# Kernel tuning notes

Hardware: AMD Instinct MI355X
Metric: run time of the kernel (lower is better)

## Reference

```python
import jax, jax.numpy as jnp
import numpy as np

N = 100000
E = 1600000
IN_FEATS = 512
N_HIDDEN = 128
N_CLASSES = 40


def setup_inputs() -> dict:
    key = jax.random.key(0)
    k1, k2, k3, k4, k5, k6, k7 = jax.random.split(key, 7)
    inputs = jax.random.normal(k1, (N, IN_FEATS), dtype=jnp.float32)
    edge_index = jax.random.randint(k2, (2, E), 0, N, dtype=jnp.int64)
    edge_attr = jax.random.uniform(k3, (E,), dtype=jnp.float32)
    # GCNConv params (Glorot-ish scaling)
    W1 = jax.random.normal(k4, (IN_FEATS, N_HIDDEN), dtype=jnp.float32) / np.sqrt(IN_FEATS)
    b1 = jnp.zeros((N_HIDDEN,), dtype=jnp.float32)
    W2 = jax.random.normal(k5, (N_HIDDEN, N_CLASSES), dtype=jnp.float32) / np.sqrt(N_HIDDEN)
    b2 = jnp.zeros((N_CLASSES,), dtype=jnp.float32)
    return {"inputs": inputs, "edge_index": edge_index, "edge_attr": edge_attr,
            "W1": W1, "b1": b1, "W2": W2, "b2": b2}


def gcn_conv(x, W, b, src, dst, edge_weight):
    """GCNConv with normalize=False: linear transform, then edge-weighted
    scatter-sum from src to dst, then bias."""
    m = x @ W                                   # [N, F_out]
    msgs = m[src] * edge_weight[:, None]        # gather + weight, [E, F_out]
    agg = jax.ops.segment_sum(msgs, dst, num_segments=x.shape[0])  # scatter-add
    return agg + b


def reference(inputs, edge_index, edge_attr, W1, b1, W2, b2):
    src, dst = edge_index[0], edge_index[1]
    h = jax.nn.relu(gcn_conv(inputs, W1, b1, src, dst, edge_attr))
    # F.dropout with training=False (eval mode) is identity -> deterministic baseline
    preds = gcn_conv(h, W2, b2, src, dst, edge_attr)
    return jax.nn.log_softmax(preds, axis=1)
```

## Files before the change

kernel.cpp:

```cpp
#include <hip/hip_runtime.h>
#include <hip/hip_bf16.h>
#include <cstdint>

#define N_NODES 100000
#define N_EDGES 1600000
#define F_IN    512
#define F_HID   128
#define F_OUT   40
#define F_OUT_PAD 48

#define BSH    8
#define NB     391
#define BEPT   8
#define BCHUNK 4096
#define GB     391
#define CONVB  140
#define FCAP   6144

typedef short v8s __attribute__((ext_vector_type(8)));
typedef float v4f __attribute__((ext_vector_type(4)));

__device__ __forceinline__ short f2bf(float f) {
    unsigned u = __float_as_uint(f);
    u += 0x7fffu + ((u >> 16) & 1u);
    return (short)(u >> 16);
}

__device__ __forceinline__ float bflo(unsigned u) { return __uint_as_float(u << 16); }
__device__ __forceinline__ float bfhi(unsigned u) { return __uint_as_float(u & 0xffff0000u); }

__device__ __forceinline__ v8s pack8(float4 a, float4 b) {
    v8s r;
    r[0] = f2bf(a.x); r[1] = f2bf(a.y); r[2] = f2bf(a.z); r[3] = f2bf(a.w);
    r[4] = f2bf(b.x); r[5] = f2bf(b.y); r[6] = f2bf(b.z); r[7] = f2bf(b.w);
    return r;
}

__device__ __forceinline__ void gload16(const void* g, void* l) {
    __builtin_amdgcn_global_load_lds(
        (const __attribute__((address_space(1))) void*)g,
        (__attribute__((address_space(3))) void*)l, 16, 0, 0);
}


__global__ __launch_bounds__(512) void k_bhist(const int* __restrict__ dst,
                                               int* __restrict__ bcnt,
                                               const float* __restrict__ W1,
                                               short* __restrict__ WT1,
                                               const float* __restrict__ W2,
                                               short* __restrict__ WT2) {
    if (blockIdx.x >= GB) {
        int i = (blockIdx.x - GB) * 512 + threadIdx.x;
        if (i < F_IN * F_HID) {
            int n = i >> 9, k = i & 511;
            WT1[i] = f2bf(W1[k * F_HID + n]);
        } else {
            int j = i - F_IN * F_HID;
            if (j < F_OUT_PAD * F_HID) {
                int n = j >> 7, k = j & 127;
                WT2[j] = (n < F_OUT) ? f2bf(W2[k * F_OUT + n]) : (short)0;
            }
        }
        return;
    }
    __shared__ int lh[512];
    int tid = threadIdx.x;
    lh[tid] = 0;
    __syncthreads();
    long e0 = (long)blockIdx.x * BCHUNK;
#pragma unroll
    for (int i = 0; i < BEPT; i++) {
        long e = e0 + tid + i * 512;
        if (e < N_EDGES) atomicAdd(&lh[dst[e] >> BSH], 1);
    }
    __syncthreads();
    if (tid < NB && lh[tid]) atomicAdd(&bcnt[tid], lh[tid]);
}

__global__ __launch_bounds__(512) void k_bscan(const int* __restrict__ bcnt,
                                               int* __restrict__ bbase,
                                               int* __restrict__ bcur) {
    __shared__ int sm[512];
    int tid = threadIdx.x;
    int v = (tid < NB) ? bcnt[tid] : 0;
    sm[tid] = v;
    __syncthreads();
    for (int off = 1; off < 512; off <<= 1) {
        int t = (tid >= off) ? sm[tid - off] : 0;
        __syncthreads();
        sm[tid] += t;
        __syncthreads();
    }
    if (tid < NB) {
        int ex = sm[tid] - v;
        bbase[tid] = ex;
        bcur[tid] = ex;
    }
    if (tid == 511) bbase[NB] = sm[511];
}

__global__ __launch_bounds__(512) void k_bscatter(const int* __restrict__ src,
                                                  const int* __restrict__ dst,
                                                  const float* __restrict__ w,
                                                  int* __restrict__ bcur,
                                                  int2* __restrict__ tmp) {
    __shared__ int cntA[512];
    __shared__ int ofsA[512];
    __shared__ int lcur[512];
    __shared__ int gb[512];
    __shared__ __align__(16) int2 recBuf[BCHUNK];
    __shared__ unsigned short bkt[BCHUNK];
    int tid = threadIdx.x;
    long e0 = (long)blockIdx.x * BCHUNK;
    cntA[tid] = 0;
    __syncthreads();

    int dloc[BEPT];
#pragma unroll
    for (int i = 0; i < BEPT; i++) {
        long e = e0 + tid + i * 512;
        int d = (e < N_EDGES) ? dst[e] : -1;
        dloc[i] = d;
        if (d >= 0) atomicAdd(&cntA[d >> BSH], 1);
    }
    __syncthreads();

    int v = cntA[tid];
    ofsA[tid] = v;
    __syncthreads();
    for (int off = 1; off < 512; off <<= 1) {
        int t = (tid >= off) ? ofsA[tid - off] : 0;
        __syncthreads();
        ofsA[tid] += t;
        __syncthreads();
    }
    int excl = ofsA[tid] - v;
    ofsA[tid] = excl;
    lcur[tid] = excl;
    if (tid < NB && v > 0) gb[tid] = atomicAdd(&bcur[tid], v);
    __syncthreads();

#pragma unroll
    for (int i = 0; i < BEPT; i++) {
        int d = dloc[i];
        if (d >= 0) {
            long e = e0 + tid + i * 512;
            int j = d >> BSH;
            int slot = atomicAdd(&lcur[j], 1);
            recBuf[slot] = make_int2(src[e] | ((d & 255) << 17), __float_as_int(w[e]));
            bkt[slot] = (unsigned short)j;
        }
    }
    __syncthreads();

    long rem = N_EDGES - e0;
    int total = (rem < BCHUNK) ? (int)rem : BCHUNK;
    for (int s = tid; s < total; s += 512) {
        int j = bkt[s];
        tmp[gb[j] + (s - ofsA[j])] = recBuf[s];
    }
}

__global__ __launch_bounds__(256) void k_fine(const int2* __restrict__ tmp,
                                              const int* __restrict__ bbase,
                                              int2* __restrict__ rec,
                                              int* __restrict__ rowptr,
                                              int* __restrict__ deg) {
    __shared__ int hist[256];
    __shared__ int ofs[256];
    __shared__ int cur[256];
    __shared__ __align__(16) int2 recOut[FCAP];
    int tid = threadIdx.x, b = blockIdx.x;
    int base = bbase[b];
    int cnt = bbase[b + 1] - base;

    hist[tid] = 0;
    __syncthreads();
    for (int i = tid; i < cnt; i += 256) {
        unsigned u = (unsigned)tmp[base + i].x;
        atomicAdd(&hist[u >> 17], 1);
    }
    __syncthreads();

    int v = hist[tid];
    ofs[tid] = v;
    __syncthreads();
    for (int off = 1; off < 256; off <<= 1) {
        int t = (tid >= off) ? ofs[tid - off] : 0;
        __syncthreads();
        ofs[tid] += t;
        __syncthreads();
    }
    int excl = ofs[tid] - v;
    ofs[tid] = excl;
    cur[tid] = excl;
    int node = (b << BSH) + tid;
    if (node < N_NODES) {
        rowptr[node] = base + excl;
        deg[node] = v;
    }
    __syncthreads();

    if (cnt <= FCAP) {
        for (int i = tid; i < cnt; i += 256) {
            int2 r = tmp[base + i];
            unsigned u = (unsigned)r.x;
            int slot = atomicAdd(&cur[u >> 17], 1);
            recOut[slot] = make_int2((int)(u & 0x1FFFFu), r.y);
        }
        __syncthreads();
        for (int i = tid; i < cnt; i += 256) rec[base + i] = recOut[i];
    } else {
        for (int i = tid; i < cnt; i += 256) {
            int2 r = tmp[base + i];
            unsigned u = (unsigned)r.x;
            int slot = atomicAdd(&cur[u >> 17], 1);
            rec[base + slot] = make_int2((int)(u & 0x1FFFFu), r.y);
        }
    }
}


__global__ __launch_bounds__(256) void k_gemm1(const float* __restrict__ x,
                                               const short* __restrict__ WT1,
                                               unsigned short* __restrict__ m1b) {
    __shared__ __align__(16) float aBuf[2][64 * 32];
    __shared__ __align__(16) short bBuf[2][128 * 32];
    int tid = threadIdx.x, w = tid >> 6, lane = tid & 63;
    int quad = lane >> 4, l16 = lane & 15;
    long rowBase = (long)blockIdx.x * 64;

    int ar = lane >> 3, ac = lane & 7;
    int br = lane >> 2, bc = lane & 3;

    v4f acc[8];
#pragma unroll
    for (int t = 0; t < 8; t++) acc[t] = (v4f){0.f, 0.f, 0.f, 0.f};

    auto stage = [&](int kc, int buf) {
#pragma unroll
        for (int i = 0; i < 2; i++) {
            int rl = w * 16 + i * 8 + ar;
            long rg = rowBase + rl;
            if (rg > N_NODES - 1) rg = N_NODES - 1;
            const float* gp = x + rg * F_IN + kc * 32 + ((ac ^ (rl & 7)) << 2);
            gload16(gp, &aBuf[buf][(w * 16 + i * 8) * 32]);
        }
#pragma unroll
        for (int i = 0; i < 2; i++) {
            int n = w * 32 + i * 16 + br;
            const short* gp = WT1 + n * F_IN + kc * 32 + ((bc ^ ((n >> 1) & 3)) << 3);
            gload16(gp, &bBuf[buf][(w * 32 + i * 16) * 32]);
        }
    };

    stage(0, 0);
#pragma unroll
    for (int kc = 0; kc < 16; kc++) {
        __syncthreads();
        int buf = kc & 1;
        if (kc < 15) stage(kc + 1, buf ^ 1);
        int arow = w * 16 + l16;
        int p0 = (2 * quad) ^ (l16 & 7);
        float4 av0 = *(const float4*)&aBuf[buf][arow * 32 + p0 * 4];
        float4 av1 = *(const float4*)&aBuf[buf][arow * 32 + (p0 ^ 1) * 4];
        v8s af = pack8(av0, av1);
#pragma unroll
        for (int t = 0; t < 8; t++) {
            int n = t * 16 + l16;
            int p = quad ^ ((n >> 1) & 3);
            v8s bf = *(const v8s*)&bBuf[buf][n * 32 + p * 8];
            acc[t] = __builtin_amdgcn_mfma_f32_16x16x32_bf16(af, bf, acc[t], 0, 0, 0);
        }
    }

#pragma unroll
    for (int t = 0; t < 8; t++)
#pragma unroll
        for (int r = 0; r < 4; r++) {
            long row = rowBase + w * 16 + quad * 4 + r;
            if (row < N_NODES)
                m1b[row * F_HID + t * 16 + l16] = (unsigned short)f2bf(acc[t][r]);
        }
}


__global__ __launch_bounds__(256) void k_ag(const int2* __restrict__ rec,
                                            const int* __restrict__ rowptr,
                                            const int* __restrict__ deg,
                                            const uint4* __restrict__ m1v,
                                            const float* __restrict__ b1,
                                            const short* __restrict__ WT2,
                                            unsigned short* __restrict__ m2b) {
    __shared__ uint4 ht[4][16][16];
    int tid = threadIdx.x, w = tid >> 6, lane = tid & 63;
    int q = lane >> 4, l16 = lane & 15;
    int gBase = (blockIdx.x * 4 + w) * 16;

    int idx = gBase + l16;
    int rp = 0, dg = 0;
    if (idx < N_NODES) { rp = rowptr[idx]; dg = deg[idx]; }
    const float4* b4 = (const float4*)b1;
    float4 bv0 = b4[2 * l16], bv1 = b4[2 * l16 + 1];

    for (int i = 0; i < 16; i++) {
        int start = __shfl(rp, i);
        int cnt = __shfl(dg, i);
        float a0 = 0.f, a1 = 0.f, a2 = 0.f, a3 = 0.f;
        float a4 = 0.f, a5 = 0.f, a6 = 0.f, a7 = 0.f;
        int e = start + q;
        int n16 = cnt >> 4;
        for (int k = 0; k < n16; k++) {
            int2 r0 = rec[e];
            int2 r1 = rec[e + 4];
            int2 r2 = rec[e + 8];
            int2 r3 = rec[e + 12];
            uint4 g0 = m1v[(long)r0.x * 16 + l16];
            uint4 g1 = m1v[(long)r1.x * 16 + l16];
            uint4 g2 = m1v[(long)r2.x * 16 + l16];
            uint4 g3 = m1v[(long)r3.x * 16 + l16];
            float w0 = __int_as_float(r0.y), w1 = __int_as_float(r1.y);
            float w2 = __int_as_float(r2.y), w3 = __int_as_float(r3.y);
            a0 = fmaf(w0, bflo(g0.x), a0); a1 = fmaf(w0, bfhi(g0.x), a1);
            a2 = fmaf(w0, bflo(g0.y), a2); a3 = fmaf(w0, bfhi(g0.y), a3);
            a4 = fmaf(w0, bflo(g0.z), a4); a5 = fmaf(w0, bfhi(g0.z), a5);
            a6 = fmaf(w0, bflo(g0.w), a6); a7 = fmaf(w0, bfhi(g0.w), a7);
            a0 = fmaf(w1, bflo(g1.x), a0); a1 = fmaf(w1, bfhi(g1.x), a1);
            a2 = fmaf(w1, bflo(g1.y), a2); a3 = fmaf(w1, bfhi(g1.y), a3);
            a4 = fmaf(w1, bflo(g1.z), a4); a5 = fmaf(w1, bfhi(g1.z), a5);
            a6 = fmaf(w1, bflo(g1.w), a6); a7 = fmaf(w1, bfhi(g1.w), a7);
            a0 = fmaf(w2, bflo(g2.x), a0); a1 = fmaf(w2, bfhi(g2.x), a1);
            a2 = fmaf(w2, bflo(g2.y), a2); a3 = fmaf(w2, bfhi(g2.y), a3);
            a4 = fmaf(w2, bflo(g2.z), a4); a5 = fmaf(w2, bfhi(g2.z), a5);
            a6 = fmaf(w2, bflo(g2.w), a6); a7 = fmaf(w2, bfhi(g2.w), a7);
            a0 = fmaf(w3, bflo(g3.x), a0); a1 = fmaf(w3, bfhi(g3.x), a1);
            a2 = fmaf(w3, bflo(g3.y), a2); a3 = fmaf(w3, bfhi(g3.y), a3);
            a4 = fmaf(w3, bflo(g3.z), a4); a5 = fmaf(w3, bfhi(g3.z), a5);
            a6 = fmaf(w3, bflo(g3.w), a6); a7 = fmaf(w3, bfhi(g3.w), a7);
            e += 16;
        }
        if (cnt & 8) {
            int2 r0 = rec[e];
            int2 r1 = rec[e + 4];
            uint4 g0 = m1v[(long)r0.x * 16 + l16];
            uint4 g1 = m1v[(long)r1.x * 16 + l16];
            float w0 = __int_as_float(r0.y), w1 = __int_as_float(r1.y);
            a0 = fmaf(w0, bflo(g0.x), a0); a1 = fmaf(w0, bfhi(g0.x), a1);
            a2 = fmaf(w0, bflo(g0.y), a2); a3 = fmaf(w0, bfhi(g0.y), a3);
            a4 = fmaf(w0, bflo(g0.z), a4); a5 = fmaf(w0, bfhi(g0.z), a5);
            a6 = fmaf(w0, bflo(g0.w), a6); a7 = fmaf(w0, bfhi(g0.w), a7);
            a0 = fmaf(w1, bflo(g1.x), a0); a1 = fmaf(w1, bfhi(g1.x), a1);
            a2 = fmaf(w1, bflo(g1.y), a2); a3 = fmaf(w1, bfhi(g1.y), a3);
            a4 = fmaf(w1, bflo(g1.z), a4); a5 = fmaf(w1, bfhi(g1.z), a5);
            a6 = fmaf(w1, bflo(g1.w), a6); a7 = fmaf(w1, bfhi(g1.w), a7);
            e += 8;
        }
        for (int t = e; t < start + cnt; t += 4) {
            int2 r = rec[t];
            uint4 g = m1v[(long)r.x * 16 + l16];
            float ww = __int_as_float(r.y);
            a0 = fmaf(ww, bflo(g.x), a0); a1 = fmaf(ww, bfhi(g.x), a1);
            a2 = fmaf(ww, bflo(g.y), a2); a3 = fmaf(ww, bfhi(g.y), a3);
            a4 = fmaf(ww, bflo(g.z), a4); a5 = fmaf(ww, bfhi(g.z), a5);
            a6 = fmaf(ww, bflo(g.w), a6); a7 = fmaf(ww, bfhi(g.w), a7);
        }
        a0 += __shfl_xor(a0, 16); a0 += __shfl_xor(a0, 32);
        a1 += __shfl_xor(a1, 16); a1 += __shfl_xor(a1, 32);
        a2 += __shfl_xor(a2, 16); a2 += __shfl_xor(a2, 32);
        a3 += __shfl_xor(a3, 16); a3 += __shfl_xor(a3, 32);
        a4 += __shfl_xor(a4, 16); a4 += __shfl_xor(a4, 32);
        a5 += __shfl_xor(a5, 16); a5 += __shfl_xor(a5, 32);
        a6 += __shfl_xor(a6, 16); a6 += __shfl_xor(a6, 32);
        a7 += __shfl_xor(a7, 16); a7 += __shfl_xor(a7, 32);
        if (q == 0) {
            a0 = fmaxf(a0 + bv0.x, 0.f); a1 = fmaxf(a1 + bv0.y, 0.f);
            a2 = fmaxf(a2 + bv0.z, 0.f); a3 = fmaxf(a3 + bv0.w, 0.f);
            a4 = fmaxf(a4 + bv1.x, 0.f); a5 = fmaxf(a5 + bv1.y, 0.f);
            a6 = fmaxf(a6 + bv1.z, 0.f); a7 = fmaxf(a7 + bv1.w, 0.f);
            uint4 o;
            o.x = (unsigned)(unsigned short)f2bf(a0) | ((unsigned)(unsigned short)f2bf(a1) << 16);
            o.y = (unsigned)(unsigned short)f2bf(a2) | ((unsigned)(unsigned short)f2bf(a3) << 16);
            o.z = (unsigned)(unsigned short)f2bf(a4) | ((unsigned)(unsigned short)f2bf(a5) << 16);
            o.w = (unsigned)(unsigned short)f2bf(a6) | ((unsigned)(unsigned short)f2bf(a7) << 16);
            ht[w][i][l16 ^ (i & 7)] = o;
        }
    }

    v4f acc[3];
#pragma unroll
    for (int t = 0; t < 3; t++) acc[t] = (v4f){0.f, 0.f, 0.f, 0.f};
#pragma unroll
    for (int kk = 0; kk < 4; kk++) {
        uint4 av = ht[w][l16][(kk * 4 + q) ^ (l16 & 7)];
        v8s af = *reinterpret_cast<const v8s*>(&av);
        const short* brow = WT2 + l16 * F_HID + q * 8 + kk * 32;
#pragma unroll
        for (int t = 0; t < 3; t++) {
            v8s bf = *reinterpret_cast<const v8s*>(brow + t * 16 * F_HID);
            acc[t] = __builtin_amdgcn_mfma_f32_16x16x32_bf16(af, bf, acc[t], 0, 0, 0);
        }
    }
#pragma unroll
    for (int r = 0; r < 4; r++) {
        int g = gBase + q * 4 + r;
        if (g < N_NODES) {
#pragma unroll
            for (int t = 0; t < 3; t++)
                m2b[(long)g * 64 + t * 16 + l16] = (unsigned short)f2bf(acc[t][r]);
            m2b[(long)g * 64 + 48 + l16] = 0;
        }
    }
}


__global__ void k_agg2(const int2* __restrict__ rec, const int* __restrict__ rowptr,
                       const int* __restrict__ deg, const uint4* __restrict__ m2v,
                       const float* __restrict__ b2, float* __restrict__ out) {
    int node = blockIdx.x * 4 + (threadIdx.x >> 6);
    int lane = threadIdx.x & 63;
    if (node >= N_NODES) return;
    int start = rowptr[node], cnt = deg[node];
    int oc = lane >> 3, l8 = lane & 7;

    float a0 = 0.f, a1 = 0.f, a2 = 0.f, a3 = 0.f;
    float a4 = 0.f, a5 = 0.f, a6 = 0.f, a7 = 0.f;

    int e = start + oc;
    int n16 = cnt >> 4;
    for (int k = 0; k < n16; k++) {
        int2 r0 = rec[e];
        int2 r1 = rec[e + 8];
        uint4 g0 = m2v[(long)r0.x * 8 + l8];
        uint4 g1 = m2v[(long)r1.x * 8 + l8];
        float w0 = __int_as_float(r0.y), w1 = __int_as_float(r1.y);
        a0 = fmaf(w0, bflo(g0.x), a0); a1 = fmaf(w0, bfhi(g0.x), a1);
        a2 = fmaf(w0, bflo(g0.y), a2); a3 = fmaf(w0, bfhi(g0.y), a3);
        a4 = fmaf(w0, bflo(g0.z), a4); a5 = fmaf(w0, bfhi(g0.z), a5);
        a6 = fmaf(w0, bflo(g0.w), a6); a7 = fmaf(w0, bfhi(g0.w), a7);
        a0 = fmaf(w1, bflo(g1.x), a0); a1 = fmaf(w1, bfhi(g1.x), a1);
        a2 = fmaf(w1, bflo(g1.y), a2); a3 = fmaf(w1, bfhi(g1.y), a3);
        a4 = fmaf(w1, bflo(g1.z), a4); a5 = fmaf(w1, bfhi(g1.z), a5);
        a6 = fmaf(w1, bflo(g1.w), a6); a7 = fmaf(w1, bfhi(g1.w), a7);
        e += 16;
    }
    if (cnt & 8) {
        int2 r = rec[e];
        uint4 g = m2v[(long)r.x * 8 + l8];
        float w = __int_as_float(r.y);
        a0 = fmaf(w, bflo(g.x), a0); a1 = fmaf(w, bfhi(g.x), a1);
        a2 = fmaf(w, bflo(g.y), a2); a3 = fmaf(w, bfhi(g.y), a3);
        a4 = fmaf(w, bflo(g.z), a4); a5 = fmaf(w, bfhi(g.z), a5);
        a6 = fmaf(w, bflo(g.w), a6); a7 = fmaf(w, bfhi(g.w), a7);
        e += 8;
    }
    if (e < start + cnt) {
        int2 r = rec[e];
        uint4 g = m2v[(long)r.x * 8 + l8];
        float w = __int_as_float(r.y);
        a0 = fmaf(w, bflo(g.x), a0); a1 = fmaf(w, bfhi(g.x), a1);
        a2 = fmaf(w, bflo(g.y), a2); a3 = fmaf(w, bfhi(g.y), a3);
        a4 = fmaf(w, bflo(g.z), a4); a5 = fmaf(w, bfhi(g.z), a5);
        a6 = fmaf(w, bflo(g.w), a6); a7 = fmaf(w, bfhi(g.w), a7);
    }
#pragma unroll
    for (int off = 8; off < 64; off <<= 1) {
        a0 += __shfl_xor(a0, off); a1 += __shfl_xor(a1, off);
        a2 += __shfl_xor(a2, off); a3 += __shfl_xor(a3, off);
        a4 += __shfl_xor(a4, off); a5 += __shfl_xor(a5, off);
        a6 += __shfl_xor(a6, off); a7 += __shfl_xor(a7, off);
    }

    const float NEG = -3.4e38f;
    float v0 = NEG, v1 = NEG, v2 = NEG, v3 = NEG;
    float v4 = NEG, v5 = NEG, v6 = NEG, v7 = NEG;
    if (l8 < 5) {
        const float4* b4 = (const float4*)b2;
        float4 bv0 = b4[2 * l8], bv1 = b4[2 * l8 + 1];
        v0 = a0 + bv0.x; v1 = a1 + bv0.y; v2 = a2 + bv0.z; v3 = a3 + bv0.w;
        v4 = a4 + bv1.x; v5 = a5 + bv1.y; v6 = a6 + bv1.z; v7 = a7 + bv1.w;
    }
    float m = fmaxf(fmaxf(fmaxf(v0, v1), fmaxf(v2, v3)),
                    fmaxf(fmaxf(v4, v5), fmaxf(v6, v7)));
#pragma unroll
    for (int off = 1; off < 8; off <<= 1) m = fmaxf(m, __shfl_xor(m, off));
    float s = 0.f;
    if (l8 < 5)
        s = __expf(v0 - m) + __expf(v1 - m) + __expf(v2 - m) + __expf(v3 - m) +
            __expf(v4 - m) + __expf(v5 - m) + __expf(v6 - m) + __expf(v7 - m);
#pragma unroll
    for (int off = 1; off < 8; off <<= 1) s += __shfl_xor(s, off);
    if (oc == 0 && l8 < 5) {
        float ls = m + __logf(s);
        float4* op = (float4*)(out + (long)node * F_OUT);
        float4 o0, o1;
        o0.x = v0 - ls; o0.y = v1 - ls; o0.z = v2 - ls; o0.w = v3 - ls;
        o1.x = v4 - ls; o1.y = v5 - ls; o1.z = v6 - ls; o1.w = v7 - ls;
        op[2 * l8] = o0;
        op[2 * l8 + 1] = o1;
    }
}


extern "C" void kernel_launch(void* const* d_in, const int* in_sizes, int n_in,
                              void* d_out, int out_size, void* d_ws, size_t ws_size,
                              hipStream_t stream) {
    const float* x  = (const float*)d_in[0];
    const int* ei   = (const int*)d_in[1];
    const int* src  = ei;
    const int* dst  = ei + N_EDGES;
    const float* ew = (const float*)d_in[2];
    const float* W1 = (const float*)d_in[3];
    const float* b1 = (const float*)d_in[4];
    const float* W2 = (const float*)d_in[5];
    const float* b2 = (const float*)d_in[6];
    float* out = (float*)d_out;

    char* ws = (char*)d_ws;
    size_t off = 0;
    auto alloc = [&](size_t bytes) {
        void* p = ws + off;
        off += (bytes + 255) & ~(size_t)255;
        return p;
    };
    unsigned short* m1b  = (unsigned short*)alloc((size_t)N_NODES * F_HID * 2);
    unsigned short* m2b  = (unsigned short*)alloc((size_t)N_NODES * 64 * 2);
    int2*           rec  = (int2*)alloc((size_t)N_EDGES * 8);
    int*          rowptr = (int*)alloc((size_t)N_NODES * 4);
    int*          deg    = (int*)alloc((size_t)N_NODES * 4);
    int*          bCnt   = (int*)alloc(512 * 4);
    int*          bBase  = (int*)alloc(512 * 4);
    int*          bCur   = (int*)alloc(512 * 4);
    short*        WT1    = (short*)alloc((size_t)F_HID * F_IN * 2);
    short*        WT2    = (short*)alloc((size_t)F_OUT_PAD * F_HID * 2);

    int2* tmp = (int2*)m2b;

    hipMemsetAsync(bCnt, 0, 512 * 4, stream);

    k_bhist<<<GB + CONVB, 512, 0, stream>>>(dst, bCnt, W1, WT1, W2, WT2);
    k_bscan<<<1, 512, 0, stream>>>(bCnt, bBase, bCur);
    k_bscatter<<<GB, 512, 0, stream>>>(src, dst, ew, bCur, tmp);
    k_fine<<<NB, 256, 0, stream>>>(tmp, bBase, rec, rowptr, deg);

    k_gemm1<<<(N_NODES + 63) / 64, 256, 0, stream>>>(x, WT1, m1b);
    k_ag<<<(N_NODES + 63) / 64, 256, 0, stream>>>(rec, rowptr, deg,
                                                  (const uint4*)m1b, b1, WT2, m2b);
    k_agg2<<<(N_NODES + 3) / 4, 256, 0, stream>>>(rec, rowptr, deg,
                                                  (const uint4*)m2b, b2, out);
}
```

Measured before the change: 491.0 us.

## Spread layer-1 aggregation across 8 waves per 16-node block, pack rowptr/deg

The layer-1 aggregation kernel is restructured. Before, each wave serially aggregated 16 nodes and then ran its own small MFMA; now a 512-thread block handles 16 nodes, with each of 8 waves aggregating 2 nodes into shared memory, and after a barrier a single wave does the W2 MFMA. The aim is more parallelism and latency hiding on the irregular gathers and less serial per-wave work. Row pointers and degrees are also packed into one int2 array so each node needs a single load. The cost is a block barrier and seven idle waves during the MFMA/store phase.

```diff
diff --git a/kernel.cpp b/kernel.cpp
--- a/kernel.cpp
+++ b/kernel.cpp
@@ -164,8 +164,7 @@
 __global__ __launch_bounds__(256) void k_fine(const int2* __restrict__ tmp,
                                               const int* __restrict__ bbase,
                                               int2* __restrict__ rec,
-                                              int* __restrict__ rowptr,
-                                              int* __restrict__ deg) {
+                                              int2* __restrict__ rd) {
     __shared__ int hist[256];
     __shared__ int ofs[256];
     __shared__ int cur[256];
@@ -195,10 +194,7 @@
     ofs[tid] = excl;
     cur[tid] = excl;
     int node = (b << BSH) + tid;
-    if (node < N_NODES) {
-        rowptr[node] = base + excl;
-        deg[node] = v;
-    }
+    if (node < N_NODES) rd[node] = make_int2(base + excl, v);
     __syncthreads();
 
     if (cnt <= FCAP) {
@@ -285,27 +281,27 @@
 }
 
 
-__global__ __launch_bounds__(256) void k_ag(const int2* __restrict__ rec,
-                                            const int* __restrict__ rowptr,
-                                            const int* __restrict__ deg,
+__global__ __launch_bounds__(512) void k_ag(const int2* __restrict__ rec,
+                                            const int2* __restrict__ rd,
                                             const uint4* __restrict__ m1v,
                                             const float* __restrict__ b1,
                                             const short* __restrict__ WT2,
                                             unsigned short* __restrict__ m2b) {
-    __shared__ uint4 ht[4][16][16];
+    __shared__ uint4 ht[16][17];
     int tid = threadIdx.x, w = tid >> 6, lane = tid & 63;
     int q = lane >> 4, l16 = lane & 15;
-    int gBase = (blockIdx.x * 4 + w) * 16;
-
-    int idx = gBase + l16;
-    int rp = 0, dg = 0;
-    if (idx < N_NODES) { rp = rowptr[idx]; dg = deg[idx]; }
+    int gBase = blockIdx.x * 16;
+
     const float4* b4 = (const float4*)b1;
     float4 bv0 = b4[2 * l16], bv1 = b4[2 * l16 + 1];
 
-    for (int i = 0; i < 16; i++) {
-        int start = __shfl(rp, i);
-        int cnt = __shfl(dg, i);
+#pragma unroll
+    for (int half = 0; half < 2; half++) {
+        int node = gBase + half * 8 + w;
+        int2 sd = make_int2(0, 0);
+        if (node < N_NODES) sd = rd[node];
+        int start = sd.x, cnt = sd.y;
+
         float a0 = 0.f, a1 = 0.f, a2 = 0.f, a3 = 0.f;
         float a4 = 0.f, a5 = 0.f, a6 = 0.f, a7 = 0.f;
         int e = start + q;
@@ -382,44 +378,48 @@
             o.y = (unsigned)(unsigned short)f2bf(a2) | ((unsigned)(unsigned short)f2bf(a3) << 16);
             o.z = (unsigned)(unsigned short)f2bf(a4) | ((unsigned)(unsigned short)f2bf(a5) << 16);
             o.w = (unsigned)(unsigned short)f2bf(a6) | ((unsigned)(unsigned short)f2bf(a7) << 16);
-            ht[w][i][l16 ^ (i & 7)] = o;
-        }
-    }
-
-    v4f acc[3];
-#pragma unroll
-    for (int t = 0; t < 3; t++) acc[t] = (v4f){0.f, 0.f, 0.f, 0.f};
-#pragma unroll
-    for (int kk = 0; kk < 4; kk++) {
-        uint4 av = ht[w][l16][(kk * 4 + q) ^ (l16 & 7)];
-        v8s af = *reinterpret_cast<const v8s*>(&av);
-        const short* brow = WT2 + l16 * F_HID + q * 8 + kk * 32;
-#pragma unroll
-        for (int t = 0; t < 3; t++) {
-            v8s bf = *reinterpret_cast<const v8s*>(brow + t * 16 * F_HID);
-            acc[t] = __builtin_amdgcn_mfma_f32_16x16x32_bf16(af, bf, acc[t], 0, 0, 0);
-        }
-    }
-#pragma unroll
-    for (int r = 0; r < 4; r++) {
-        int g = gBase + q * 4 + r;
-        if (g < N_NODES) {
-#pragma unroll
-            for (int t = 0; t < 3; t++)
-                m2b[(long)g * 64 + t * 16 + l16] = (unsigned short)f2bf(acc[t][r]);
-            m2b[(long)g * 64 + 48 + l16] = 0;
-        }
-    }
-}
-
-
-__global__ void k_agg2(const int2* __restrict__ rec, const int* __restrict__ rowptr,
-                       const int* __restrict__ deg, const uint4* __restrict__ m2v,
-                       const float* __restrict__ b2, float* __restrict__ out) {
+            ht[half * 8 + w][l16] = o;
+        }
+    }
+    __syncthreads();
+
+    if (w == 0) {
+        v4f acc[3];
+#pragma unroll
+        for (int t = 0; t < 3; t++) acc[t] = (v4f){0.f, 0.f, 0.f, 0.f};
+#pragma unroll
+        for (int kk = 0; kk < 4; kk++) {
+            uint4 av = ht[l16][kk * 4 + q];
+            v8s af = *reinterpret_cast<const v8s*>(&av);
+            const short* brow = WT2 + l16 * F_HID + q * 8 + kk * 32;
+#pragma unroll
+            for (int t = 0; t < 3; t++) {
+                v8s bf = *reinterpret_cast<const v8s*>(brow + t * 16 * F_HID);
+                acc[t] = __builtin_amdgcn_mfma_f32_16x16x32_bf16(af, bf, acc[t], 0, 0, 0);
+            }
+        }
+#pragma unroll
+        for (int r = 0; r < 4; r++) {
+            int g = gBase + q * 4 + r;
+            if (g < N_NODES) {
+#pragma unroll
+                for (int t = 0; t < 3; t++)
+                    m2b[(long)g * 64 + t * 16 + l16] = (unsigned short)f2bf(acc[t][r]);
+                m2b[(long)g * 64 + 48 + l16] = 0;
+            }
+        }
+    }
+}
+
+
+__global__ void k_agg2(const int2* __restrict__ rec, const int2* __restrict__ rd,
+                       const uint4* __restrict__ m2v, const float* __restrict__ b2,
+                       float* __restrict__ out) {
     int node = blockIdx.x * 4 + (threadIdx.x >> 6);
     int lane = threadIdx.x & 63;
     if (node >= N_NODES) return;
-    int start = rowptr[node], cnt = deg[node];
+    int2 sd = rd[node];
+    int start = sd.x, cnt = sd.y;
     int oc = lane >> 3, l8 = lane & 7;
 
     float a0 = 0.f, a1 = 0.f, a2 = 0.f, a3 = 0.f;
@@ -525,8 +525,7 @@
     unsigned short* m1b  = (unsigned short*)alloc((size_t)N_NODES * F_HID * 2);
     unsigned short* m2b  = (unsigned short*)alloc((size_t)N_NODES * 64 * 2);
     int2*           rec  = (int2*)alloc((size_t)N_EDGES * 8);
-    int*          rowptr = (int*)alloc((size_t)N_NODES * 4);
-    int*          deg    = (int*)alloc((size_t)N_NODES * 4);
+    int2*           rd   = (int2*)alloc((size_t)N_NODES * 8);
     int*          bCnt   = (int*)alloc(512 * 4);
     int*          bBase  = (int*)alloc(512 * 4);
     int*          bCur   = (int*)alloc(512 * 4);
@@ -540,11 +539,11 @@
     k_bhist<<<GB + CONVB, 512, 0, stream>>>(dst, bCnt, W1, WT1, W2, WT2);
     k_bscan<<<1, 512, 0, stream>>>(bCnt, bBase, bCur);
     k_bscatter<<<GB, 512, 0, stream>>>(src, dst, ew, bCur, tmp);
-    k_fine<<<NB, 256, 0, stream>>>(tmp, bBase, rec, rowptr, deg);
+    k_fine<<<NB, 256, 0, stream>>>(tmp, bBase, rec, rd);
 
     k_gemm1<<<(N_NODES + 63) / 64, 256, 0, stream>>>(x, WT1, m1b);
-    k_ag<<<(N_NODES + 63) / 64, 256, 0, stream>>>(rec, rowptr, deg,
-                                                  (const uint4*)m1b, b1, WT2, m2b);
-    k_agg2<<<(N_NODES + 3) / 4, 256, 0, stream>>>(rec, rowptr, deg,
-                                                  (const uint4*)m2b, b2, out);
-}
+    k_ag<<<(N_NODES + 15) / 16, 512, 0, stream>>>(rec, rd, (const uint4*)m1b,
+                                                  b1, WT2, m2b);
+    k_agg2<<<(N_NODES + 3) / 4, 256, 0, stream>>>(rec, rd, (const uint4*)m2b,
+                                                  b2, out);
+}
```

After: 484.0 us. About the same (-1.4%).
